# Optimization experiments

Measured on AMD Instinct MI355X. Metric: run time of the kernel, lower is better.

Reference implementation:

```python
import jax, jax.numpy as jnp
import numpy as np

EPS = 1e-6

def _ln(x, g, b):
    mu = jnp.mean(x, axis=-1, keepdims=True)
    var = jnp.mean(jnp.square(x - mu), axis=-1, keepdims=True)
    return (x - mu) * jax.lax.rsqrt(var + EPS) * g + b

def setup_inputs() -> dict:
    key = jax.random.key(0)
    ks = jax.random.split(key, 8)
    B, S, D, H, HD, F = 4, 1024, 1024, 16, 64, 4096
    s = 0.02
    return {
        "hidden_state": jax.random.normal(ks[0], (B, S, D), jnp.float32),
        "mask": jnp.ones((B, S), jnp.int32),
        "Wq": jax.random.normal(ks[1], (H, D, HD), jnp.float32) * s,
        "bq": jnp.zeros((H, HD), jnp.float32),
        "Wk": jax.random.normal(ks[2], (H, D, HD), jnp.float32) * s,
        "bk": jnp.zeros((H, HD), jnp.float32),
        "Wv": jax.random.normal(ks[3], (H, D, HD), jnp.float32) * s,
        "bv": jnp.zeros((H, HD), jnp.float32),
        "Wo": jax.random.normal(ks[4], (D, D), jnp.float32) * s,
        "bo": jnp.zeros((D,), jnp.float32),
        "ln1_g": jnp.ones((D,), jnp.float32),
        "ln1_b": jnp.zeros((D,), jnp.float32),
        "ln2_g": jnp.ones((D,), jnp.float32),
        "ln2_b": jnp.zeros((D,), jnp.float32),
        "W1": jax.random.normal(ks[5], (D, F), jnp.float32) * s,
        "b1": jnp.zeros((F,), jnp.float32),
        "W2": jax.random.normal(ks[6], (F, D), jnp.float32) * s,
        "b2": jnp.zeros((D,), jnp.float32),
    }

def reference(hidden_state, mask, Wq, bq, Wk, bk, Wv, bv, Wo, bo,
              ln1_g, ln1_b, ln2_g, ln2_b, W1, b1, W2, b2):
    # Pre-norm
    x1 = _ln(hidden_state, ln1_g, ln1_b)  # [B,S,D]
    # Per-head projections stacked over head axis h
    q = jnp.einsum('bsd,hdk->bhsk', x1, Wq) + bq[:, None, :]
    k = jnp.einsum('bsd,hdk->bhsk', x1, Wk) + bk[:, None, :]
    v = jnp.einsum('bsd,hdk->bhsk', x1, Wv) + bv[:, None, :]
    head_dim = q.shape[-1]
    scores = jnp.einsum('bhqk,bhsk->bhqs', q, k) / jnp.sqrt(jnp.float32(head_dim))
    scores = jnp.where(mask[:, None, None, :] == 0, jnp.float32(-1e9), scores)
    w = jax.nn.softmax(scores, axis=-1)
    attn = jnp.einsum('bhqs,bhsk->bhqk', w, v)  # [B,H,S,HD]
    B, H, S, HD = attn.shape
    attn = attn.transpose(0, 2, 1, 3).reshape(B, S, H * HD)  # concat heads
    attn = attn @ Wo + bo
    h = attn + hidden_state
    x2 = _ln(h, ln2_g, ln2_b)
    ff = jax.nn.gelu(x2 @ W1 + b1, approximate=False) @ W2 + b2
    return ff + h
```

## Files before the change

### kernel.cpp

```cpp
#include <hip/hip_runtime.h>

typedef __bf16 bf16;
typedef __bf16 bf16x4 __attribute__((ext_vector_type(4)));
typedef __bf16 bf16x8 __attribute__((ext_vector_type(8)));
typedef float  f32x4  __attribute__((ext_vector_type(4)));

#define F32X4_ZERO ((f32x4){0.f, 0.f, 0.f, 0.f})

__device__ __forceinline__ f32x4 mfma16(bf16x8 a, bf16x8 b, f32x4 c) {
  return __builtin_amdgcn_mfma_f32_16x16x32_bf16(a, b, c, 0, 0, 0);
}

__device__ __forceinline__ void gld16(const void* g, void* l) {
  __builtin_amdgcn_global_load_lds((const __attribute__((address_space(1))) void*)g,
                                   (__attribute__((address_space(3))) void*)l, 16, 0, 0);
}

__device__ __forceinline__ float gelu_f(float u) {
  return 0.5f * u * (1.0f + erff(u * 0.70710678118654752f));
}

__device__ __forceinline__ bf16x8 frag_ld(const bf16* base, int row, int c16) {
  return *(const bf16x8*)((const char*)base + row * 128 + (((c16) ^ (row & 7)) << 4));
}

__device__ __forceinline__ int fo32(int row, int c16) {
  return row * 64 + ((c16 ^ ((row >> 1) & 3)) << 4);
}
#define WAITB(N) asm volatile("s_waitcnt vmcnt(" #N ")\ns_barrier" ::: "memory")

__global__ void transpose2(const float* __restrict__ src, size_t sBatch, int sStride,
                           bf16* __restrict__ dst, size_t dBatch, int dStride) {
  __shared__ bf16 t[32][33];
  src += (size_t)blockIdx.z * sBatch;
  dst += (size_t)blockIdx.z * dBatch;
  int c0 = blockIdx.x * 32, r0 = blockIdx.y * 32;
#pragma unroll
  for (int i = 0; i < 4; i++) {
    int r = threadIdx.y + i * 8;
    t[r][threadIdx.x] = (bf16)src[(size_t)(r0 + r) * sStride + c0 + threadIdx.x];
  }
  __syncthreads();
#pragma unroll
  for (int i = 0; i < 4; i++) {
    int c = threadIdx.y + i * 8;
    dst[(size_t)(c0 + c) * dStride + r0 + threadIdx.x] = t[threadIdx.x][c];
  }
}

__global__ __launch_bounds__(256) void ln_rows(const float* __restrict__ in,
                                               const float* __restrict__ gam,
                                               const float* __restrict__ bet,
                                               bf16* __restrict__ out) {
  int row = blockIdx.x, tid = threadIdx.x;
  f32x4 x = *(const f32x4*)(in + (size_t)row * 1024 + tid * 4);
  float s = 0.f, q = 0.f;
#pragma unroll
  for (int j = 0; j < 4; j++) { s += x[j]; q += x[j] * x[j]; }
#pragma unroll
  for (int o = 1; o < 64; o <<= 1) {
    s += __shfl_xor(s, o, 64);
    q += __shfl_xor(q, o, 64);
  }
  __shared__ float red[8];
  if ((tid & 63) == 0) { red[(tid >> 6) * 2] = s; red[(tid >> 6) * 2 + 1] = q; }
  __syncthreads();
  s = red[0] + red[2] + red[4] + red[6];
  q = red[1] + red[3] + red[5] + red[7];
  float mean = s * (1.f / 1024.f);
  float var  = q * (1.f / 1024.f) - mean * mean;
  float inv  = rsqrtf(var + 1e-6f);
  bf16x4 o;
#pragma unroll
  for (int j = 0; j < 4; j++) {
    int c = tid * 4 + j;
    o[j] = (bf16)((x[j] - mean) * inv * gam[c] + bet[c]);
  }
  *(bf16x4*)(out + (size_t)row * 1024 + tid * 4) = o;
}

enum { EPI_WO = 0, EPI_GELU = 1, EPI_ACC0 = 2, EPI_ACC = 3, EPI_FINAL = 4 };

__global__ __launch_bounds__(512) void pipe256x128_gelu(
    const bf16* __restrict__ A, const bf16* __restrict__ BT, const float* __restrict__ bias,
    int N, bf16* __restrict__ outb) {
  int tid = threadIdx.x, lane = tid & 63, wv = tid >> 6;
  int bid = blockIdx.x;
  int xcd = bid & 7, idx = bid >> 3;
  int m0 = ((xcd >> 1) * 4 + (idx >> 4)) * 256;
  int n0 = ((xcd & 1) * 16 + (idx & 15)) * 128;
  int wrow = (wv >> 1) * 64, wcol = (wv & 1) * 64;
  __shared__ __align__(16) bf16 lds[3][12288];
  f32x4 acc[4][4];
#pragma unroll
  for (int a = 0; a < 4; a++)
#pragma unroll
    for (int n = 0; n < 4; n++) acc[a][n] = F32X4_ZERO;

  constexpr int K = 1024, nk = K / 32;
  int rin = lane >> 2;
  int sbc = ((lane & 3) ^ ((lane >> 3) & 3)) * 16;
  const char* gsrc[3]; int ldof[3];
#pragma unroll
  for (int j = 0; j < 3; j++) {
    int c = wv * 3 + j;
    if (c < 16) gsrc[j] = (const char*)A  + ((size_t)(m0 + c * 16 + rin) * K) * 2 + sbc;
    else        gsrc[j] = (const char*)BT + ((size_t)(n0 + (c - 16) * 16 + rin) * K) * 2 + sbc;
    ldof[j] = c * 1024;
  }
  auto stage = [&](int slot) {
#pragma unroll
    for (int j = 0; j < 3; j++) {
      gld16(gsrc[j], (char*)lds[slot] + ldof[j]);
      gsrc[j] += 64;
    }
  };
  int c16 = lane >> 4;
  int foA[4], foB[4];
#pragma unroll
  for (int mf = 0; mf < 4; mf++) foA[mf] = fo32(wrow + mf * 16 + (lane & 15), c16);
#pragma unroll
  for (int nf = 0; nf < 4; nf++) foB[nf] = 16384 + fo32(wcol + nf * 16 + (lane & 15), c16);

  stage(0); stage(1);
#pragma unroll 1
  for (int t = 0; t < nk; t++) {
    if (t < nk - 1) WAITB(3);
    else            WAITB(0);
    if (t + 2 < nk) stage((t + 2) % 3);
    const char* sb = (const char*)lds[t % 3];
    bf16x8 af[4], bfr[4];
#pragma unroll
    for (int mf = 0; mf < 4; mf++) af[mf] = *(const bf16x8*)(sb + foA[mf]);
#pragma unroll
    for (int nf = 0; nf < 4; nf++) bfr[nf] = *(const bf16x8*)(sb + foB[nf]);
#pragma unroll
    for (int mf = 0; mf < 4; mf++)
#pragma unroll
      for (int nf = 0; nf < 4; nf++)
        acc[mf][nf] = mfma16(af[mf], bfr[nf], acc[mf][nf]);
  }
#pragma unroll
  for (int mf = 0; mf < 4; mf++)
#pragma unroll
    for (int nf = 0; nf < 4; nf++)
#pragma unroll
      for (int i = 0; i < 4; i++) {
        int row = m0 + wrow + mf * 16 + ((lane >> 4) << 2) + i;
        int col = n0 + wcol + nf * 16 + (lane & 15);
        outb[(size_t)row * N + col] = (bf16)gelu_f(acc[mf][nf][i] + bias[col]);
      }
}

__global__ __launch_bounds__(512) void qkv_pipe256(
    const bf16* __restrict__ x1,
    const bf16* __restrict__ WqT, const bf16* __restrict__ WkT, const bf16* __restrict__ WvT,
    const float* __restrict__ bq, const float* __restrict__ bk, const float* __restrict__ bv,
    bf16* __restrict__ qo, bf16* __restrict__ ko, bf16* __restrict__ vto) {
  int tid = threadIdx.x, lane = tid & 63, wv = tid >> 6;
  int z = blockIdx.z;
  const bf16* BT; const float* bias;
  if (z == 0)      { BT = WqT; bias = bq; }
  else if (z == 1) { BT = WkT; bias = bk; }
  else             { BT = WvT; bias = bv; }
  int bid = blockIdx.x;
  int xcd = bid & 7, idx = bid >> 3;
  int m0 = (xcd * 2 + (idx >> 3)) * 256;
  int n0 = (idx & 7) * 128;
  int wrow = (wv >> 1) * 64, wcol = (wv & 1) * 64;
  __shared__ __align__(16) bf16 lds[3][12288];
  f32x4 acc[4][4];
#pragma unroll
  for (int a = 0; a < 4; a++)
#pragma unroll
    for (int n = 0; n < 4; n++) acc[a][n] = F32X4_ZERO;

  constexpr int K = 1024, nk = K / 32;
  int rin = lane >> 2;
  int sbc = ((lane & 3) ^ ((lane >> 3) & 3)) * 16;
  const char* gsrc[3]; int ldof[3];
#pragma unroll
  for (int j = 0; j < 3; j++) {
    int c = wv * 3 + j;
    if (c < 16) gsrc[j] = (const char*)x1 + ((size_t)(m0 + c * 16 + rin) * K) * 2 + sbc;
    else        gsrc[j] = (const char*)BT + ((size_t)(n0 + (c - 16) * 16 + rin) * K) * 2 + sbc;
    ldof[j] = c * 1024;
  }
  auto stage = [&](int slot) {
#pragma unroll
    for (int j = 0; j < 3; j++) {
      gld16(gsrc[j], (char*)lds[slot] + ldof[j]);
      gsrc[j] += 64;
    }
  };
  int c16 = lane >> 4;
  int foA[4], foB[4];
#pragma unroll
  for (int mf = 0; mf < 4; mf++) foA[mf] = fo32(wrow + mf * 16 + (lane & 15), c16);
#pragma unroll
  for (int nf = 0; nf < 4; nf++) foB[nf] = 16384 + fo32(wcol + nf * 16 + (lane & 15), c16);

  stage(0); stage(1);
#pragma unroll 1
  for (int t = 0; t < nk; t++) {
    if (t < nk - 1) WAITB(3);
    else            WAITB(0);
    if (t + 2 < nk) stage((t + 2) % 3);
    const char* sb = (const char*)lds[t % 3];
    bf16x8 af[4], bfr[4];
#pragma unroll
    for (int mf = 0; mf < 4; mf++) af[mf] = *(const bf16x8*)(sb + foA[mf]);
#pragma unroll
    for (int nf = 0; nf < 4; nf++) bfr[nf] = *(const bf16x8*)(sb + foB[nf]);
#pragma unroll
    for (int mf = 0; mf < 4; mf++)
#pragma unroll
      for (int nf = 0; nf < 4; nf++)
        acc[mf][nf] = mfma16(af[mf], bfr[nf], acc[mf][nf]);
  }
#pragma unroll
  for (int mf = 0; mf < 4; mf++)
#pragma unroll
    for (int nf = 0; nf < 4; nf++)
#pragma unroll
      for (int i = 0; i < 4; i++) {
        int row  = m0 + wrow + mf * 16 + ((lane >> 4) << 2) + i;
        int ncol = n0 + wcol + nf * 16 + (lane & 15);
        int bb = row >> 10, s = row & 1023, head = ncol >> 6, d = ncol & 63;
        size_t bh = (size_t)bb * 16 + head;
        float v = acc[mf][nf][i] + bias[ncol];
        if (z == 0)      qo[(bh * 1024 + s) * 64 + d] = (bf16)(v * 0.125f);
        else if (z == 1) ko[(bh * 1024 + s) * 64 + d] = (bf16)v;
        else             vto[(bh * 64 + d) * 1024 + s] = (bf16)v;
      }
}

template <int EPI, int K, int NTL, int DEPTH>
__global__ __launch_bounds__(256) void pipe128(
    const bf16* __restrict__ A, const bf16* __restrict__ BT, const float* __restrict__ bias,
    int N,
    const float* __restrict__ resid, float* __restrict__ facc,
    bf16* __restrict__ outb, float* __restrict__ outf) {
  int tid = threadIdx.x, lane = tid & 63, wv = tid >> 6;
  int bid = blockIdx.x + (blockIdx.y << 3);
  int xcd = bid & 7, idx = bid >> 3;
  int m0 = (xcd * 4 + (idx >> NTL)) * 128;
  int n0 = (idx & ((1 << NTL) - 1)) * 128;
  int wrow = (wv >> 1) * 64, wcol = (wv & 1) * 64;
  constexpr int SLOTS = DEPTH + 1;
  __shared__ __align__(16) bf16 lds[SLOTS][8192];
  f32x4 acc[4][4];
#pragma unroll
  for (int a = 0; a < 4; a++)
#pragma unroll
    for (int n = 0; n < 4; n++) acc[a][n] = F32X4_ZERO;

  constexpr int nk = K / 32;
  int rin = lane >> 2;
  int sbc = ((lane & 3) ^ ((lane >> 3) & 3)) * 16;
  const char* gsrc[4]; int ldof[4];
#pragma unroll
  for (int j = 0; j < 4; j++) {
    int c = wv * 4 + j;
    if (c < 8) gsrc[j] = (const char*)A  + ((size_t)(m0 + c * 16 + rin) * K) * 2 + sbc;
    else       gsrc[j] = (const char*)BT + ((size_t)(n0 + (c - 8) * 16 + rin) * K) * 2 + sbc;
    ldof[j] = c * 1024;
  }
  auto stage = [&](int slot) {
#pragma unroll
    for (int j = 0; j < 4; j++) {
      gld16(gsrc[j], (char*)lds[slot] + ldof[j]);
      gsrc[j] += 64;
    }
  };
  int c16 = lane >> 4;
  int foA[4], foB[4];
#pragma unroll
  for (int mf = 0; mf < 4; mf++) foA[mf] = fo32(wrow + mf * 16 + (lane & 15), c16);
#pragma unroll
  for (int nf = 0; nf < 4; nf++) foB[nf] = 8192 + fo32(wcol + nf * 16 + (lane & 15), c16);

#pragma unroll
  for (int p = 0; p < DEPTH; p++) stage(p);
#pragma unroll 1
  for (int t = 0; t < nk; t++) {
    if constexpr (DEPTH == 2) {
      if (t < nk - 1) WAITB(4);
      else            WAITB(0);
    } else {
      if (t < nk - 2)       WAITB(8);
      else if (t == nk - 2) WAITB(4);
      else                  WAITB(0);
    }
    if (t + DEPTH < nk) stage((t + DEPTH) % SLOTS);
    const char* sb = (const char*)lds[t % SLOTS];
    bf16x8 af[4], bfr[4];
#pragma unroll
    for (int mf = 0; mf < 4; mf++) af[mf] = *(const bf16x8*)(sb + foA[mf]);
#pragma unroll
    for (int nf = 0; nf < 4; nf++) bfr[nf] = *(const bf16x8*)(sb + foB[nf]);
#pragma unroll
    for (int mf = 0; mf < 4; mf++)
#pragma unroll
      for (int nf = 0; nf < 4; nf++)
        acc[mf][nf] = mfma16(af[mf], bfr[nf], acc[mf][nf]);
  }
#pragma unroll
  for (int mf = 0; mf < 4; mf++)
#pragma unroll
    for (int nf = 0; nf < 4; nf++)
#pragma unroll
      for (int i = 0; i < 4; i++) {
        int row = m0 + wrow + mf * 16 + ((lane >> 4) << 2) + i;
        int col = n0 + wcol + nf * 16 + (lane & 15);
        size_t idx2 = (size_t)row * N + col;
        float v = acc[mf][nf][i];
        if constexpr (EPI == EPI_WO) {
          outf[idx2] = v + bias[col] + resid[idx2];
        } else if constexpr (EPI == EPI_GELU) {
          outb[idx2] = (bf16)gelu_f(v + bias[col]);
        } else if constexpr (EPI == EPI_ACC0) {
          facc[idx2] = v;
        } else if constexpr (EPI == EPI_ACC) {
          facc[idx2] += v;
        } else {
          outf[idx2] = facc[idx2] + v + bias[col] + resid[idx2];
        }
      }
}

__global__ __launch_bounds__(512) void attn_flash(
    const bf16* __restrict__ qb, const bf16* __restrict__ kb, const bf16* __restrict__ vtb,
    const int* __restrict__ mask, bf16* __restrict__ attnC) {
  int tid = threadIdx.x, lane = tid & 63, wv = tid >> 6;
  int wgid = blockIdx.x;
  int nid  = (wgid & 7) * 64 + (wgid >> 3);
  int qblk = nid & 7, h = (nid >> 3) & 15, b = nid >> 7;
  int qrow0 = qblk * 128 + wv * 16;

  __shared__ float smask[1024];
  __shared__ __align__(16) bf16 kt[2][64 * 64];
  __shared__ __align__(16) bf16 vt[2][64 * 64];
  __shared__ __align__(16) bf16 pb[8][16][72];
  for (int i = tid; i < 1024; i += 512) smask[i] = mask[b * 1024 + i] ? 0.f : -1e9f;

  size_t bh = (size_t)b * 16 + h;
  const bf16* qp = qb + (bh * 1024 + qrow0) * 64;
  bf16x8 qa[2];
#pragma unroll
  for (int kc = 0; kc < 2; kc++)
    qa[kc] = *(const bf16x8*)(qp + (lane & 15) * 64 + kc * 32 + (lane >> 4) * 8);

  const bf16* kp = kb + bh * 1024 * 64;
  const bf16* vp = vtb + bh * 64 * 1024;
  bf16* myp = &pb[wv][0][0];

  bf16x8 vone;
#pragma unroll
  for (int j = 0; j < 8; j++) vone[j] = (bf16)1.0f;

  f32x4 ssum = F32X4_ZERO;
  f32x4 oacc[4];
#pragma unroll
  for (int i = 0; i < 4; i++) oacc[i] = F32X4_ZERO;

  int srl = lane >> 3;
  int sbc = ((lane & 7) ^ srl) * 16;
  auto stage = [&](int buf, int t2) {
    int key0n = t2 * 64;
#pragma unroll
    for (int j = 0; j < 2; j++) {
      int c = wv * 2 + j;
      if (c < 8) {
        int row = c * 8 + srl;
        gld16((const char*)kp + ((size_t)(key0n + row) * 64) * 2 + sbc,
              (char*)kt[buf] + c * 1024);
      } else {
        int row = (c - 8) * 8 + srl;
        gld16((const char*)vp + ((size_t)row * 1024 + key0n) * 2 + sbc,
              (char*)vt[buf] + (c - 8) * 1024);
      }
    }
  };

  stage(0, 0);
  __syncthreads();

  for (int t = 0; t < 16; t++) {
    int cur = t & 1;
    if (t < 15) stage(cur ^ 1, t + 1);
    const bf16* kcur = kt[cur];
    const bf16* vcur = vt[cur];
    int key0 = t * 64;
    f32x4 st[4];
    __builtin_amdgcn_s_setprio(1);
#pragma unroll
    for (int nt = 0; nt < 4; nt++) {
      st[nt] = F32X4_ZERO;
#pragma unroll
      for (int kc = 0; kc < 2; kc++) {
        bf16x8 kf = frag_ld(kcur, nt * 16 + (lane & 15), kc * 4 + (lane >> 4));
        st[nt] = mfma16(qa[kc], kf, st[nt]);
      }
    }
    __builtin_amdgcn_s_setprio(0);
#pragma unroll
    for (int nt = 0; nt < 4; nt++) {
      float ms = smask[key0 + nt * 16 + (lane & 15)] - 8.0f;
#pragma unroll
      for (int i = 0; i < 4; i++) st[nt][i] = __expf(st[nt][i] + ms);
    }
#pragma unroll
    for (int nt = 0; nt < 4; nt++)
#pragma unroll
      for (int i = 0; i < 4; i++)
        myp[((lane >> 4) * 4 + i) * 72 + nt * 16 + (lane & 15)] = (bf16)st[nt][i];
    __builtin_amdgcn_s_setprio(1);
#pragma unroll
    for (int kc = 0; kc < 2; kc++) {
      bf16x8 pa = *(const bf16x8*)(myp + (lane & 15) * 72 + kc * 32 + (lane >> 4) * 8);
      ssum = mfma16(pa, vone, ssum);
#pragma unroll
      for (int dn = 0; dn < 4; dn++) {
        bf16x8 vf = frag_ld(vcur, dn * 16 + (lane & 15), kc * 4 + (lane >> 4));
        oacc[dn] = mfma16(pa, vf, oacc[dn]);
      }
    }
    __builtin_amdgcn_s_setprio(0);
    __syncthreads();
  }
#pragma unroll
  for (int i = 0; i < 4; i++) {
    float inv = 1.0f / ssum[i];
    int row = qrow0 + ((lane >> 4) << 2) + i;
#pragma unroll
    for (int dn = 0; dn < 4; dn++)
      attnC[(size_t)(b * 1024 + row) * 1024 + h * 64 + dn * 16 + (lane & 15)] =
          (bf16)(oacc[dn][i] * inv);
  }
}

template <int EPI, int K>
__global__ __launch_bounds__(256) void gemm_bt(
    const bf16* __restrict__ A, const bf16* __restrict__ BT, const float* __restrict__ bias,
    int N,
    const float* __restrict__ resid, float* __restrict__ facc,
    bf16* __restrict__ outb, float* __restrict__ outf) {
  int tid = threadIdx.x, lane = tid & 63, wv = tid >> 6;
  int m0 = blockIdx.y * 128, n0 = blockIdx.x * 128;
  int wrow = (wv >> 1) * 64, wcol = (wv & 1) * 64;
  __shared__ __align__(16) bf16 lA[2][128 * 64];
  __shared__ __align__(16) bf16 lB[2][128 * 64];
  f32x4 acc[4][4];
#pragma unroll
  for (int a = 0; a < 4; a++)
#pragma unroll
    for (int n = 0; n < 4; n++) acc[a][n] = F32X4_ZERO;

  int cbs = ((lane & 7) ^ (lane >> 3)) * 16;
  auto stage = [&](int buf, int k0) {
#pragma unroll
    for (int s = 0; s < 4; s++) {
      int c = s * 4 + wv;
      int row = c * 8 + (lane >> 3);
      gld16((const char*)A  + ((size_t)(m0 + row) * K + k0) * 2 + cbs,
            (char*)lA[buf] + c * 1024);
      gld16((const char*)BT + ((size_t)(n0 + row) * K + k0) * 2 + cbs,
            (char*)lB[buf] + c * 1024);
    }
  };

  constexpr int nk = K >> 6;
  stage(0, 0);
  __syncthreads();
#pragma unroll 1
  for (int t = 0; t < nk; t++) {
    int cur = t & 1;
    if (t + 1 < nk) stage(cur ^ 1, (t + 1) * 64);
#pragma unroll
    for (int kc = 0; kc < 2; kc++) {
      int c16 = kc * 4 + (lane >> 4);
      bf16x8 af[4], bfr[4];
#pragma unroll
      for (int mf = 0; mf < 4; mf++)
        af[mf] = frag_ld(lA[cur], wrow + mf * 16 + (lane & 15), c16);
#pragma unroll
      for (int nf = 0; nf < 4; nf++)
        bfr[nf] = frag_ld(lB[cur], wcol + nf * 16 + (lane & 15), c16);
#pragma unroll
      for (int mf = 0; mf < 4; mf++)
#pragma unroll
        for (int nf = 0; nf < 4; nf++)
          acc[mf][nf] = mfma16(af[mf], bfr[nf], acc[mf][nf]);
    }
    __syncthreads();
  }
#pragma unroll
  for (int mf = 0; mf < 4; mf++)
#pragma unroll
    for (int nf = 0; nf < 4; nf++)
#pragma unroll
      for (int i = 0; i < 4; i++) {
        int row = m0 + wrow + mf * 16 + ((lane >> 4) << 2) + i;
        int col = n0 + wcol + nf * 16 + (lane & 15);
        size_t idx2 = (size_t)row * N + col;
        float v = acc[mf][nf][i];
        if constexpr (EPI == EPI_WO) {
          outf[idx2] = v + bias[col] + resid[idx2];
        } else if constexpr (EPI == EPI_GELU) {
          outb[idx2] = (bf16)gelu_f(v + bias[col]);
        } else if constexpr (EPI == EPI_ACC0) {
          facc[idx2] = v;
        } else if constexpr (EPI == EPI_ACC) {
          facc[idx2] += v;
        } else {
          outf[idx2] = facc[idx2] + v + bias[col] + resid[idx2];
        }
      }
}

extern "C" void kernel_launch(void* const* d_in, const int* in_sizes, int n_in,
                              void* d_out, int out_size, void* d_ws, size_t ws_size,
                              hipStream_t stream) {
  const float* hidden = (const float*)d_in[0];
  const int*   mask   = (const int*)d_in[1];
  const float* Wq = (const float*)d_in[2];
  const float* bq = (const float*)d_in[3];
  const float* Wk = (const float*)d_in[4];
  const float* bk = (const float*)d_in[5];
  const float* Wv = (const float*)d_in[6];
  const float* bv = (const float*)d_in[7];
  const float* Wo = (const float*)d_in[8];
  const float* bo = (const float*)d_in[9];
  const float* ln1g = (const float*)d_in[10];
  const float* ln1b = (const float*)d_in[11];
  const float* ln2g = (const float*)d_in[12];
  const float* ln2b = (const float*)d_in[13];
  const float* W1 = (const float*)d_in[14];
  const float* b1 = (const float*)d_in[15];
  const float* W2 = (const float*)d_in[16];
  const float* b2 = (const float*)d_in[17];
  float* out = (float*)d_out;

  char* ws = (char*)d_ws;
  const size_t MB = 1ull << 20;
  dim3 tb(32, 8);
  const size_t HB = 64 * 1024;

  if (ws_size >= 96 * MB) {
    bf16* x1    = (bf16*)(ws + 0 * MB);
    bf16* attnC = x1;
    bf16* x2    = x1;
    bf16* qbuf  = (bf16*)(ws + 8 * MB);
    bf16* W1T   = qbuf;
    bf16* kbuf  = (bf16*)(ws + 16 * MB);
    bf16* W2T   = kbuf;
    bf16* vtbuf = (bf16*)(ws + 24 * MB);
    float* hbuf = (float*)(ws + 32 * MB);
    bf16* WqT   = (bf16*)(ws + 48 * MB);
    bf16* WkT   = (bf16*)(ws + 50 * MB);
    bf16* WvT   = (bf16*)(ws + 52 * MB);
    bf16* WoT   = (bf16*)(ws + 54 * MB);
    bf16* gbuf  = (bf16*)(ws + 56 * MB);

    transpose2<<<dim3(2, 32, 16), tb, 0, stream>>>(Wq, HB, 64, WqT, HB, 1024);
    transpose2<<<dim3(2, 32, 16), tb, 0, stream>>>(Wk, HB, 64, WkT, HB, 1024);
    transpose2<<<dim3(2, 32, 16), tb, 0, stream>>>(Wv, HB, 64, WvT, HB, 1024);
    transpose2<<<dim3(32, 32, 1), tb, 0, stream>>>(Wo, 0, 1024, WoT, 0, 1024);
    ln_rows<<<4096, 256, 0, stream>>>(hidden, ln1g, ln1b, x1);
    qkv_pipe256<<<dim3(128, 1, 3), 512, 0, stream>>>(x1, WqT, WkT, WvT, bq, bk, bv,
                                                     qbuf, kbuf, vtbuf);
    attn_flash<<<512, 512, 0, stream>>>(qbuf, kbuf, vtbuf, mask, attnC);
    pipe128<EPI_WO, 1024, 3, 3><<<dim3(8, 32), 256, 0, stream>>>(attnC, WoT, bo, 1024,
                                                                 hidden, nullptr, nullptr, hbuf);
    ln_rows<<<4096, 256, 0, stream>>>(hbuf, ln2g, ln2b, x2);
    transpose2<<<dim3(128, 32, 1), tb, 0, stream>>>(W1, 0, 4096, W1T, 0, 1024);
    transpose2<<<dim3(32, 128, 1), tb, 0, stream>>>(W2, 0, 1024, W2T, 0, 4096);
    pipe256x128_gelu<<<512, 512, 0, stream>>>(x2, W1T, b1, 4096, gbuf);
    pipe128<EPI_WO, 4096, 3, 3><<<dim3(8, 32), 256, 0, stream>>>(gbuf, W2T, b2, 1024,
                                                                 hbuf, nullptr, nullptr, out);
  } else {
    bf16* x1     = (bf16*)(ws + 0 * MB);
    bf16* attnC  = x1;
    bf16* x2     = x1;
    bf16* qbuf   = (bf16*)(ws + 8 * MB);
    bf16* W1Tc   = (bf16*)(ws + 8 * MB);
    bf16* W2Tc   = (bf16*)(ws + 10 * MB);
    bf16* gchunk = (bf16*)(ws + 12 * MB);
    bf16* kbuf   = (bf16*)(ws + 16 * MB);
    bf16* vtbuf  = (bf16*)(ws + 24 * MB);
    float* hbuf  = (float*)(ws + 16 * MB);
    bf16* WqT    = (bf16*)(ws + 32 * MB);
    bf16* WkT    = (bf16*)(ws + 34 * MB);
    bf16* WvT    = (bf16*)(ws + 36 * MB);
    bf16* WoT    = (bf16*)(ws + 38 * MB);
    float* outacc = (float*)(ws + 40 * MB);

    transpose2<<<dim3(2, 32, 16), tb, 0, stream>>>(Wq, HB, 64, WqT, HB, 1024);
    transpose2<<<dim3(2, 32, 16), tb, 0, stream>>>(Wk, HB, 64, WkT, HB, 1024);
    transpose2<<<dim3(2, 32, 16), tb, 0, stream>>>(Wv, HB, 64, WvT, HB, 1024);
    transpose2<<<dim3(32, 32, 1), tb, 0, stream>>>(Wo, 0, 1024, WoT, 0, 1024);
    ln_rows<<<4096, 256, 0, stream>>>(hidden, ln1g, ln1b, x1);
    qkv_pipe256<<<dim3(128, 1, 3), 512, 0, stream>>>(x1, WqT, WkT, WvT, bq, bk, bv,
                                                     qbuf, kbuf, vtbuf);
    attn_flash<<<512, 512, 0, stream>>>(qbuf, kbuf, vtbuf, mask, attnC);
    pipe128<EPI_WO, 1024, 3, 3><<<dim3(8, 32), 256, 0, stream>>>(attnC, WoT, bo, 1024,
                                                                 hidden, nullptr, nullptr, hbuf);
    ln_rows<<<4096, 256, 0, stream>>>(hbuf, ln2g, ln2b, x2);

    for (int c = 0; c < 8; c++) {
      transpose2<<<dim3(16, 32, 1), tb, 0, stream>>>(W1 + c * 512, 0, 4096,
                                                     W1Tc, 0, 1024);
      transpose2<<<dim3(32, 16, 1), tb, 0, stream>>>(W2 + (size_t)c * 512 * 1024, 0, 1024,
                                                     W2Tc, 0, 512);
      gemm_bt<EPI_GELU, 1024><<<dim3(4, 32), 256, 0, stream>>>(x2, W1Tc, b1 + c * 512, 512,
                                                               nullptr, nullptr, gchunk, nullptr);
      if (c == 0)
        gemm_bt<EPI_ACC0, 512><<<dim3(8, 32), 256, 0, stream>>>(gchunk, W2Tc, b2, 1024,
                                                                nullptr, outacc, nullptr, nullptr);
      else if (c < 7)
        gemm_bt<EPI_ACC, 512><<<dim3(8, 32), 256, 0, stream>>>(gchunk, W2Tc, b2, 1024,
                                                               nullptr, outacc, nullptr, nullptr);
      else
        gemm_bt<EPI_FINAL, 512><<<dim3(8, 32), 256, 0, stream>>>(gchunk, W2Tc, b2, 1024,
                                                                 hbuf, outacc, nullptr, out);
    }
  }

  (void)in_sizes; (void)n_in; (void)out_size;
}
```

Measured before the change: 227.5 us.

## Use square 256x256 tiles for the GELU GEMM and revert pipe128 to depth two

```diff
diff --git a/kernel.cpp b/kernel.cpp
--- a/kernel.cpp
+++ b/kernel.cpp
@@ -81,67 +81,67 @@
 
 enum { EPI_WO = 0, EPI_GELU = 1, EPI_ACC0 = 2, EPI_ACC = 3, EPI_FINAL = 4 };
 
-__global__ __launch_bounds__(512) void pipe256x128_gelu(
+__global__ __launch_bounds__(512) void pipe256sq_gelu(
     const bf16* __restrict__ A, const bf16* __restrict__ BT, const float* __restrict__ bias,
     int N, bf16* __restrict__ outb) {
   int tid = threadIdx.x, lane = tid & 63, wv = tid >> 6;
   int bid = blockIdx.x;
   int xcd = bid & 7, idx = bid >> 3;
-  int m0 = ((xcd >> 1) * 4 + (idx >> 4)) * 256;
-  int n0 = ((xcd & 1) * 16 + (idx & 15)) * 128;
-  int wrow = (wv >> 1) * 64, wcol = (wv & 1) * 64;
-  __shared__ __align__(16) bf16 lds[3][12288];
-  f32x4 acc[4][4];
-#pragma unroll
-  for (int a = 0; a < 4; a++)
+  int m0 = ((xcd >> 1) * 4 + (idx >> 3)) * 256;
+  int n0 = ((xcd & 1) * 8 + (idx & 7)) * 256;
+  int wrow = (wv >> 2) * 128, wcol = (wv & 3) * 64;
+  __shared__ __align__(16) bf16 lds[3][16384];
+  f32x4 acc[8][4];
+#pragma unroll
+  for (int a = 0; a < 8; a++)
 #pragma unroll
     for (int n = 0; n < 4; n++) acc[a][n] = F32X4_ZERO;
 
   constexpr int K = 1024, nk = K / 32;
   int rin = lane >> 2;
   int sbc = ((lane & 3) ^ ((lane >> 3) & 3)) * 16;
-  const char* gsrc[3]; int ldof[3];
-#pragma unroll
-  for (int j = 0; j < 3; j++) {
-    int c = wv * 3 + j;
+  const char* gsrc[4]; int ldof[4];
+#pragma unroll
+  for (int j = 0; j < 4; j++) {
+    int c = wv * 4 + j;
     if (c < 16) gsrc[j] = (const char*)A  + ((size_t)(m0 + c * 16 + rin) * K) * 2 + sbc;
     else        gsrc[j] = (const char*)BT + ((size_t)(n0 + (c - 16) * 16 + rin) * K) * 2 + sbc;
     ldof[j] = c * 1024;
   }
   auto stage = [&](int slot) {
 #pragma unroll
-    for (int j = 0; j < 3; j++) {
+    for (int j = 0; j < 4; j++) {
       gld16(gsrc[j], (char*)lds[slot] + ldof[j]);
       gsrc[j] += 64;
     }
   };
   int c16 = lane >> 4;
-  int foA[4], foB[4];
-#pragma unroll
-  for (int mf = 0; mf < 4; mf++) foA[mf] = fo32(wrow + mf * 16 + (lane & 15), c16);
+  int foA[8], foB[4];
+#pragma unroll
+  for (int mf = 0; mf < 8; mf++) foA[mf] = fo32(wrow + mf * 16 + (lane & 15), c16);
 #pragma unroll
   for (int nf = 0; nf < 4; nf++) foB[nf] = 16384 + fo32(wcol + nf * 16 + (lane & 15), c16);
 
   stage(0); stage(1);
 #pragma unroll 1
   for (int t = 0; t < nk; t++) {
-    if (t < nk - 1) WAITB(3);
+    if (t < nk - 1) WAITB(4);
     else            WAITB(0);
     if (t + 2 < nk) stage((t + 2) % 3);
     const char* sb = (const char*)lds[t % 3];
-    bf16x8 af[4], bfr[4];
-#pragma unroll
-    for (int mf = 0; mf < 4; mf++) af[mf] = *(const bf16x8*)(sb + foA[mf]);
+    bf16x8 bfr[4];
 #pragma unroll
     for (int nf = 0; nf < 4; nf++) bfr[nf] = *(const bf16x8*)(sb + foB[nf]);
 #pragma unroll
-    for (int mf = 0; mf < 4; mf++)
+    for (int mf = 0; mf < 8; mf++) {
+      bf16x8 af = *(const bf16x8*)(sb + foA[mf]);
 #pragma unroll
       for (int nf = 0; nf < 4; nf++)
-        acc[mf][nf] = mfma16(af[mf], bfr[nf], acc[mf][nf]);
-  }
-#pragma unroll
-  for (int mf = 0; mf < 4; mf++)
+        acc[mf][nf] = mfma16(af, bfr[nf], acc[mf][nf]);
+    }
+  }
+#pragma unroll
+  for (int mf = 0; mf < 8; mf++)
 #pragma unroll
     for (int nf = 0; nf < 4; nf++)
 #pragma unroll
@@ -235,7 +235,7 @@
       }
 }
 
-template <int EPI, int K, int NTL, int DEPTH>
+template <int EPI, int K, int NTL>
 __global__ __launch_bounds__(256) void pipe128(
     const bf16* __restrict__ A, const bf16* __restrict__ BT, const float* __restrict__ bias,
     int N,
@@ -247,8 +247,7 @@
   int m0 = (xcd * 4 + (idx >> NTL)) * 128;
   int n0 = (idx & ((1 << NTL) - 1)) * 128;
   int wrow = (wv >> 1) * 64, wcol = (wv & 1) * 64;
-  constexpr int SLOTS = DEPTH + 1;
-  __shared__ __align__(16) bf16 lds[SLOTS][8192];
+  __shared__ __align__(16) bf16 lds[3][8192];
   f32x4 acc[4][4];
 #pragma unroll
   for (int a = 0; a < 4; a++)
@@ -280,20 +279,13 @@
 #pragma unroll
   for (int nf = 0; nf < 4; nf++) foB[nf] = 8192 + fo32(wcol + nf * 16 + (lane & 15), c16);
 
-#pragma unroll
-  for (int p = 0; p < DEPTH; p++) stage(p);
+  stage(0); stage(1);
 #pragma unroll 1
   for (int t = 0; t < nk; t++) {
-    if constexpr (DEPTH == 2) {
-      if (t < nk - 1) WAITB(4);
-      else            WAITB(0);
-    } else {
-      if (t < nk - 2)       WAITB(8);
-      else if (t == nk - 2) WAITB(4);
-      else                  WAITB(0);
-    }
-    if (t + DEPTH < nk) stage((t + DEPTH) % SLOTS);
-    const char* sb = (const char*)lds[t % SLOTS];
+    if (t < nk - 1) WAITB(4);
+    else            WAITB(0);
+    if (t + 2 < nk) stage((t + 2) % 3);
+    const char* sb = (const char*)lds[t % 3];
     bf16x8 af[4], bfr[4];
 #pragma unroll
     for (int mf = 0; mf < 4; mf++) af[mf] = *(const bf16x8*)(sb + foA[mf]);
@@ -571,14 +563,14 @@
     qkv_pipe256<<<dim3(128, 1, 3), 512, 0, stream>>>(x1, WqT, WkT, WvT, bq, bk, bv,
                                                      qbuf, kbuf, vtbuf);
     attn_flash<<<512, 512, 0, stream>>>(qbuf, kbuf, vtbuf, mask, attnC);
-    pipe128<EPI_WO, 1024, 3, 3><<<dim3(8, 32), 256, 0, stream>>>(attnC, WoT, bo, 1024,
-                                                                 hidden, nullptr, nullptr, hbuf);
+    pipe128<EPI_WO, 1024, 3><<<dim3(8, 32), 256, 0, stream>>>(attnC, WoT, bo, 1024,
+                                                              hidden, nullptr, nullptr, hbuf);
     ln_rows<<<4096, 256, 0, stream>>>(hbuf, ln2g, ln2b, x2);
     transpose2<<<dim3(128, 32, 1), tb, 0, stream>>>(W1, 0, 4096, W1T, 0, 1024);
     transpose2<<<dim3(32, 128, 1), tb, 0, stream>>>(W2, 0, 1024, W2T, 0, 4096);
-    pipe256x128_gelu<<<512, 512, 0, stream>>>(x2, W1T, b1, 4096, gbuf);
-    pipe128<EPI_WO, 4096, 3, 3><<<dim3(8, 32), 256, 0, stream>>>(gbuf, W2T, b2, 1024,
-                                                                 hbuf, nullptr, nullptr, out);
+    pipe256sq_gelu<<<256, 512, 0, stream>>>(x2, W1T, b1, 4096, gbuf);
+    pipe128<EPI_WO, 4096, 3><<<dim3(8, 32), 256, 0, stream>>>(gbuf, W2T, b2, 1024,
+                                                              hbuf, nullptr, nullptr, out);
   } else {
     bf16* x1     = (bf16*)(ws + 0 * MB);
     bf16* attnC  = x1;
@@ -604,8 +596,8 @@
     qkv_pipe256<<<dim3(128, 1, 3), 512, 0, stream>>>(x1, WqT, WkT, WvT, bq, bk, bv,
                                                      qbuf, kbuf, vtbuf);
     attn_flash<<<512, 512, 0, stream>>>(qbuf, kbuf, vtbuf, mask, attnC);
-    pipe128<EPI_WO, 1024, 3, 3><<<dim3(8, 32), 256, 0, stream>>>(attnC, WoT, bo, 1024,
-                                                                 hidden, nullptr, nullptr, hbuf);
+    pipe128<EPI_WO, 1024, 3><<<dim3(8, 32), 256, 0, stream>>>(attnC, WoT, bo, 1024,
+                                                              hidden, nullptr, nullptr, hbuf);
     ln_rows<<<4096, 256, 0, stream>>>(hbuf, ln2g, ln2b, x2);
 
     for (int c = 0; c < 8; c++) {
```

New measurement: 256.4 us. 1.13x slower.
